# Kernel tuning notes

Hardware: AMD Instinct MI355X
Metric: run time of the kernel (lower is better)

Reference implementation:

```python
import jax, jax.numpy as jnp
import numpy as np

EMB_DIM = 1024
NUM_HEADS = 16
DEPTH = EMB_DIM // NUM_HEADS
B, LQ, LKV = 2, 1024, 2048


def setup_inputs() -> dict:
    key = jax.random.key(0)
    ks = jax.random.split(key, 8)
    s = 1.0 / np.sqrt(EMB_DIM)
    return {
        "x": jax.random.normal(ks[0], (B, LQ, EMB_DIM), jnp.float32),
        "context": jax.random.normal(ks[1], (B, LKV, EMB_DIM), jnp.float32),
        "pad_mask": jax.random.bernoulli(ks[2], 0.1, (B, LQ, LKV)),
        "Wq": jax.random.normal(ks[3], (EMB_DIM, EMB_DIM), jnp.float32) * s,
        "Wk": jax.random.normal(ks[4], (EMB_DIM, EMB_DIM), jnp.float32) * s,
        "Wv": jax.random.normal(ks[5], (EMB_DIM, EMB_DIM), jnp.float32) * s,
        "fc_w": jax.random.normal(ks[6], (EMB_DIM, EMB_DIM), jnp.float32) * s,
        "fc_b": jax.random.normal(ks[7], (EMB_DIM,), jnp.float32) * s,
    }


def reference(x, context, pad_mask, Wq, Wk, Wv, fc_w, fc_b):
    # Projections (torch Linear: y = x @ W.T)
    Q = jnp.einsum("bqe,fe->bqf", x, Wq)
    K = jnp.einsum("bke,fe->bkf", context, Wk)
    V = jnp.einsum("bke,fe->bkf", context, Wv)
    # Split heads: [B, H, L, D]
    Q = Q.reshape(B, LQ, NUM_HEADS, DEPTH).transpose(0, 2, 1, 3)
    K = K.reshape(B, LKV, NUM_HEADS, DEPTH).transpose(0, 2, 1, 3)
    V = V.reshape(B, LKV, NUM_HEADS, DEPTH).transpose(0, 2, 1, 3)
    # Scaled dot-product attention scores [B, H, LQ, LKV]
    scores = jnp.einsum("bhqd,bhkd->bhqk", Q, K) / np.sqrt(DEPTH).astype(np.float32)
    scores = jnp.where(pad_mask[:, None, :, :], jnp.float32(-1e9), scores)
    att = jax.nn.softmax(scores, axis=-1)
    out = jnp.einsum("bhqk,bhkd->bhqd", att, V)
    out = out.transpose(0, 2, 1, 3).reshape(B, LQ, EMB_DIM)
    return jnp.einsum("bqe,fe->bqf", out, fc_w) + fc_b
```

## Files before the change

### kernel.cpp

```cpp
#include <hip/hip_runtime.h>
#include <hip/hip_bf16.h>

#define B_   2
#define H_   16
#define LQ_  1024
#define LKV_ 2048
#define D_   64
#define E_   1024

typedef __attribute__((ext_vector_type(8))) _Float16 f16x8;
typedef __attribute__((ext_vector_type(4))) float   f32x4;

__device__ __forceinline__ void gload16_lds(const void* g, void* l) {
    __builtin_amdgcn_global_load_lds(
        (const __attribute__((address_space(1))) unsigned int*)g,
        (__attribute__((address_space(3))) unsigned int*)l, 16, 0, 0);
}

__global__ void probe14(const void* __restrict__ msk, int* __restrict__ modep) {
    int lane = threadIdx.x;
    int notInt = 0, notF32 = 0, notBF = 0;
    for (int i = lane; i < 256; i += 64) {
        unsigned v = ((const unsigned*)msk)[i * 997];
        if (v > 1u) notInt = 1;
        if (v != 0u && v != 0x3F800000u) notF32 = 1;
        if (v != 0u && v != 0x3F80u && v != 0x3F800000u && v != 0x3F803F80u) notBF = 1;
    }
    notInt = __any(notInt); notF32 = __any(notF32); notBF = __any(notBF);
    if (lane == 0) *modep = !notInt ? 0 : (!notF32 ? 1 : (!notBF ? 2 : 3));
}

__global__ void canon14_all(
    const float* __restrict__ x,  const float* __restrict__ ctx,
    const float* __restrict__ wq, const float* __restrict__ wk,
    const float* __restrict__ wv, const float* __restrict__ fw,
    const float* __restrict__ fb, const void* __restrict__ msk,
    _Float16* __restrict__ xh,  _Float16* __restrict__ ch,
    _Float16* __restrict__ wqh, _Float16* __restrict__ wkvh,
    _Float16* __restrict__ fwh, float* __restrict__ fbf,
    unsigned long long* __restrict__ Mbt, const int* __restrict__ modep)
{
    const int mmode = *modep;
    const int total = 1376384;
    const int stride = gridDim.x * blockDim.x;
    for (int idx = blockIdx.x * blockDim.x + threadIdx.x; idx < total; idx += stride) {
        if (idx < 1310720) {
            const float* src; _Float16* dst; int rel;
            if (idx < 262144)       { src = x;   dst = xh;   rel = idx; }
            else if (idx < 786432)  { src = ctx; dst = ch;   rel = idx - 262144; }
            else if (idx < 917504)  { src = wq;  dst = wqh;  rel = idx - 786432; }
            else if (idx < 1048576) { src = wk;  dst = wkvh; rel = idx - 917504; }
            else if (idx < 1179648) { src = wv;  dst = wkvh + (size_t)E_ * E_; rel = idx - 1048576; }
            else                    { src = fw;  dst = fwh;  rel = idx - 1179648; }
            f32x4 a = ((const f32x4*)src)[2 * rel], b = ((const f32x4*)src)[2 * rel + 1];
            f16x8 o;
            o[0] = (_Float16)a.x; o[1] = (_Float16)a.y; o[2] = (_Float16)a.z; o[3] = (_Float16)a.w;
            o[4] = (_Float16)b.x; o[5] = (_Float16)b.y; o[6] = (_Float16)b.z; o[7] = (_Float16)b.w;
            ((f16x8*)dst)[rel] = o;
        } else if (idx < 1310848) {
            int rel = idx - 1310720;
#pragma unroll
            for (int j = 0; j < 8; ++j) fbf[rel * 8 + j] = fb[rel * 8 + j];
        } else {
            int rel = idx - 1310848;
            const size_t base = (size_t)rel * 64;
            unsigned long long v = 0;
            if (mmode == 0) {
                const int* p = (const int*)msk + base;
#pragma unroll
                for (int j = 0; j < 64; ++j) if (p[j] != 0) v |= 1ull << j;
            } else if (mmode == 1) {
                const float* p = (const float*)msk + base;
#pragma unroll
                for (int j = 0; j < 64; ++j) if (p[j] != 0.0f) v |= 1ull << j;
            } else if (mmode == 2) {
                const unsigned short* p = (const unsigned short*)msk + base;
#pragma unroll
                for (int j = 0; j < 64; ++j) if (p[j] != 0) v |= 1ull << j;
            } else {
                const unsigned char* p = (const unsigned char*)msk + base;
#pragma unroll
                for (int j = 0; j < 64; ++j) if (p[j] != 0) v |= 1ull << j;
            }
            Mbt[(rel & 31) * 2048 + (rel >> 5)] = v;
        }
    }
}

__global__ __launch_bounds__(256) void gemm14_qkv(
    const _Float16* __restrict__ xh, const _Float16* __restrict__ ch,
    const _Float16* __restrict__ wqh, const _Float16* __restrict__ wkvh,
    _Float16* __restrict__ Qh, _Float16* __restrict__ Kh, _Float16* __restrict__ Vt)
{
    __shared__ __align__(16) _Float16 As[128 * 64];
    __shared__ __align__(16) _Float16 Bs[128 * 64];

    const int bid = blockIdx.x;
    const bool isQ = bid < 128;
    const _Float16* A; const _Float16* W; int tm, tn;
    if (isQ) { A = xh; W = wqh; tm = bid >> 3; tn = bid & 7; }
    else     { int b2 = bid - 128; A = ch; W = wkvh; tm = b2 >> 4; tn = b2 & 15; }

    const int tid = threadIdx.x;
    const int w = tid >> 6, lane = tid & 63;
    const int g = lane >> 4, c = lane & 15;
    const int wr = w >> 1, wc = w & 1;
    const int rowS = lane >> 3, slot = lane & 7;
    const int stSwz = ((slot ^ (rowS & 7)) << 4);
    const int swz0 = ((g ^ (c & 7)) << 4);
    const int swz1 = (((4 + g) ^ (c & 7)) << 4);

    f32x4 acc[4][4];
#pragma unroll
    for (int i = 0; i < 4; i++)
#pragma unroll
        for (int j = 0; j < 4; j++) acc[i][j] = f32x4{0.f, 0.f, 0.f, 0.f};

    const size_t rowB = (size_t)E_ * 2;
    const char* gAbase = (const char*)A + (size_t)(tm * 128) * rowB;
    const char* gBbase = (const char*)W + (size_t)(tn * 128) * rowB;

    for (int kt = 0; kt < 16; ++kt) {
#pragma unroll
        for (int j = 0; j < 4; ++j) {
            int rloc = w * 32 + j * 8 + rowS;
            gload16_lds(gAbase + (size_t)rloc * rowB + kt * 128 + stSwz,
                        (char*)As + (w * 32 + j * 8) * 128 + lane * 16);
            gload16_lds(gBbase + (size_t)rloc * rowB + kt * 128 + stSwz,
                        (char*)Bs + (w * 32 + j * 8) * 128 + lane * 16);
        }
        __syncthreads();

        f16x8 bF[4][2];
#pragma unroll
        for (int ni = 0; ni < 4; ni++) {
            const char* bp = (const char*)Bs + (wc * 64 + ni * 16 + c) * 128;
            bF[ni][0] = *(const f16x8*)(bp + swz0);
            bF[ni][1] = *(const f16x8*)(bp + swz1);
        }
#pragma unroll
        for (int mi = 0; mi < 4; mi++) {
            const char* ap = (const char*)As + (wr * 64 + mi * 16 + c) * 128;
            f16x8 a0 = *(const f16x8*)(ap + swz0);
            f16x8 a1 = *(const f16x8*)(ap + swz1);
#pragma unroll
            for (int ni = 0; ni < 4; ni++) {
                acc[mi][ni] = __builtin_amdgcn_mfma_f32_16x16x32_f16(a0, bF[ni][0], acc[mi][ni], 0, 0, 0);
                acc[mi][ni] = __builtin_amdgcn_mfma_f32_16x16x32_f16(a1, bF[ni][1], acc[mi][ni], 0, 0, 0);
            }
        }
        __syncthreads();
    }

#pragma unroll
    for (int mi = 0; mi < 4; mi++) {
#pragma unroll
        for (int ni = 0; ni < 4; ni++) {
#pragma unroll
            for (int r = 0; r < 4; r++) {
                int R  = tm * 128 + wr * 64 + mi * 16 + g * 4 + r;
                int Cc = tn * 128 + wc * 64 + ni * 16 + c;
                float v = acc[mi][ni][r];
                if (isQ) {
                    int b = R >> 10, q = R & 1023;
                    int h = Cc >> 6, d = Cc & 63;
                    Qh[((size_t)(b * H_ + h) * LQ_ + q) * D_ + d] = (_Float16)(v * 0.18033688011112042f);
                } else {
                    int b = R >> 11, k = R & 2047;
                    int isV = Cc >> 10, cc2 = Cc & 1023;
                    int h = cc2 >> 6, d = cc2 & 63;
                    if (!isV)
                        Kh[((size_t)(b * H_ + h) * LKV_ + k) * D_ + d] = (_Float16)v;
                    else {
                        size_t bh = (size_t)(b * H_ + h);
                        Vt[((bh * (LKV_ / 64) + (k >> 6)) * D_ + d) * 64 + (k & 63)] = (_Float16)v;
                    }
                }
            }
        }
    }
}

__global__ __launch_bounds__(256) void gemm14_fc(
    const _Float16* __restrict__ A, const _Float16* __restrict__ W,
    const float* __restrict__ bias, float* __restrict__ Cout)
{
    __shared__ __align__(16) _Float16 As[128 * 64];
    __shared__ __align__(16) _Float16 Bs[128 * 64];

    const int tm = blockIdx.x >> 3, tn = blockIdx.x & 7;
    const int tid = threadIdx.x;
    const int w = tid >> 6, lane = tid & 63;
    const int g = lane >> 4, c = lane & 15;
    const int wr = w >> 1, wc = w & 1;
    const int rowS = lane >> 3, slot = lane & 7;
    const int stSwz = ((slot ^ (rowS & 7)) << 4);
    const int swz0 = ((g ^ (c & 7)) << 4);
    const int swz1 = (((4 + g) ^ (c & 7)) << 4);

    f32x4 acc[4][4];
#pragma unroll
    for (int i = 0; i < 4; i++)
#pragma unroll
        for (int j = 0; j < 4; j++) acc[i][j] = f32x4{0.f, 0.f, 0.f, 0.f};

    const size_t rowB = (size_t)E_ * 2;
    const char* gAbase = (const char*)A + (size_t)(tm * 128) * rowB;
    const char* gBbase = (const char*)W + (size_t)(tn * 128) * rowB;

    for (int kt = 0; kt < 16; ++kt) {
#pragma unroll
        for (int j = 0; j < 4; ++j) {
            int rloc = w * 32 + j * 8 + rowS;
            gload16_lds(gAbase + (size_t)rloc * rowB + kt * 128 + stSwz,
                        (char*)As + (w * 32 + j * 8) * 128 + lane * 16);
            gload16_lds(gBbase + (size_t)rloc * rowB + kt * 128 + stSwz,
                        (char*)Bs + (w * 32 + j * 8) * 128 + lane * 16);
        }
        __syncthreads();

        f16x8 bF[4][2];
#pragma unroll
        for (int ni = 0; ni < 4; ni++) {
            const char* bp = (const char*)Bs + (wc * 64 + ni * 16 + c) * 128;
            bF[ni][0] = *(const f16x8*)(bp + swz0);
            bF[ni][1] = *(const f16x8*)(bp + swz1);
        }
#pragma unroll
        for (int mi = 0; mi < 4; mi++) {
            const char* ap = (const char*)As + (wr * 64 + mi * 16 + c) * 128;
            f16x8 a0 = *(const f16x8*)(ap + swz0);
            f16x8 a1 = *(const f16x8*)(ap + swz1);
#pragma unroll
            for (int ni = 0; ni < 4; ni++) {
                acc[mi][ni] = __builtin_amdgcn_mfma_f32_16x16x32_f16(a0, bF[ni][0], acc[mi][ni], 0, 0, 0);
                acc[mi][ni] = __builtin_amdgcn_mfma_f32_16x16x32_f16(a1, bF[ni][1], acc[mi][ni], 0, 0, 0);
            }
        }
        __syncthreads();
    }

#pragma unroll
    for (int mi = 0; mi < 4; mi++)
#pragma unroll
        for (int ni = 0; ni < 4; ni++)
#pragma unroll
            for (int r = 0; r < 4; r++) {
                int R  = tm * 128 + wr * 64 + mi * 16 + g * 4 + r;
                int Cc = tn * 128 + wc * 64 + ni * 16 + c;
                Cout[(size_t)R * E_ + Cc] = acc[mi][ni][r] + bias[Cc];
            }
}

__global__ __launch_bounds__(256) void attn14_kernel(
    const _Float16* __restrict__ Qh,
    const _Float16* __restrict__ Kh,
    const _Float16* __restrict__ Vt,
    const unsigned long long* __restrict__ Mbt,
    _Float16* __restrict__ O)
{
    __shared__ __align__(16) char ldsraw[32768];

    const int bid0 = blockIdx.x;
    const int xcd = bid0 & 7, jj = bid0 >> 3;
    const int bh = xcd * 4 + (jj >> 4);
    const int qt = jj & 15;
    const int b = bh >> 4, h = bh & 15;
    const int tid = threadIdx.x;
    const int w = tid >> 6, lane = tid & 63;
    const int g = lane >> 4, c = lane & 15;
    const int q0 = qt * 64 + w * 16;

    f16x8 qf[2];
#pragma unroll
    for (int ks = 0; ks < 2; ++ks)
        qf[ks] = *(const f16x8*)&Qh[((size_t)bh * LQ_ + q0 + c) * D_ + ks * 32 + g * 8];

    f32x4 o[4];
#pragma unroll
    for (int dt = 0; dt < 4; dt++) o[dt] = f32x4{0.f, 0.f, 0.f, 0.f};
    float m = -1e30f, lsum = 0.f;

    const int rowS = (lane >> 3);
    const int stOffBase = (rowS * 128) + (((lane & 7) ^ (rowS & 7)) * 16);
    const char* kTile0 = (const char*)Kh + (size_t)bh * (LKV_ * D_ * 2);
    const char* vTile0 = (const char*)Vt + (size_t)bh * (LKV_ * D_ * 2);

    int rdOff[2];
#pragma unroll
    for (int ks = 0; ks < 2; ++ks)
        rdOff[ks] = c * 128 + (((ks * 4 + g) ^ (c & 7)) * 16);

    const int srcLo = (((g & 1) << 1) * 16 + c) << 2;
    const int srcHi = ((((g & 1) << 1) + 1) * 16 + c) << 2;
    const bool hiSel = (g >= 2);

    const int mRowIdx = b * LQ_ + q0 + c;

    {
#pragma unroll
        for (int j = 0; j < 2; ++j) {
            gload16_lds(kTile0 + (w * 2048 + j * 1024) + stOffBase, ldsraw + (w * 2048 + j * 1024));
            gload16_lds(vTile0 + (w * 2048 + j * 1024) + stOffBase, ldsraw + 8192 + (w * 2048 + j * 1024));
        }
    }
    __syncthreads();

    for (int t = 0; t < 32; ++t) {
        if (t < 31) {
            const char* kt = kTile0 + (size_t)(t + 1) * 8192;
            const char* vt = vTile0 + (size_t)(t + 1) * 8192;
            char* dst = ldsraw + ((t + 1) & 1) * 16384;
#pragma unroll
            for (int j = 0; j < 2; ++j) {
                gload16_lds(kt + (w * 2048 + j * 1024) + stOffBase, dst + (w * 2048 + j * 1024));
                gload16_lds(vt + (w * 2048 + j * 1024) + stOffBase, dst + 8192 + (w * 2048 + j * 1024));
            }
        }

        const char* bufp = ldsraw + (t & 1) * 16384;

        f32x4 s[4];
#pragma unroll
        for (int nt = 0; nt < 4; ++nt) {
            f32x4 accS = f32x4{0.f, 0.f, 0.f, 0.f};
#pragma unroll
            for (int ks = 0; ks < 2; ++ks) {
                f16x8 kf = *(const f16x8*)(bufp + nt * 2048 + rdOff[ks]);
                accS = __builtin_amdgcn_mfma_f32_16x16x32_f16(kf, qf[ks], accS, 0, 0, 0);
            }
            s[nt] = accS;
        }
        unsigned long long mks = Mbt[(size_t)t * 2048 + mRowIdx] >> (g * 4);
#pragma unroll
        for (int nt = 0; nt < 4; ++nt) {
            unsigned nib = (unsigned)(mks >> (nt * 16)) & 0xFu;
            if (nib & 1u) s[nt][0] = -1e9f;
            if (nib & 2u) s[nt][1] = -1e9f;
            if (nib & 4u) s[nt][2] = -1e9f;
            if (nib & 8u) s[nt][3] = -1e9f;
        }
        float t0 = fmaxf(fmaxf(s[0][0], s[0][1]), fmaxf(s[0][2], s[0][3]));
        float t1 = fmaxf(fmaxf(s[1][0], s[1][1]), fmaxf(s[1][2], s[1][3]));
        float t2 = fmaxf(fmaxf(s[2][0], s[2][1]), fmaxf(s[2][2], s[2][3]));
        float t3 = fmaxf(fmaxf(s[3][0], s[3][1]), fmaxf(s[3][2], s[3][3]));
        float tmax = fmaxf(fmaxf(t0, t1), fmaxf(t2, t3));
        tmax = fmaxf(tmax, __shfl_xor(tmax, 16, 64));
        tmax = fmaxf(tmax, __shfl_xor(tmax, 32, 64));
        float mn = fmaxf(m, tmax);
        float scl = exp2f(m - mn);
        m = mn;
        float ts = 0.f;
#pragma unroll
        for (int nt = 0; nt < 4; ++nt) {
            float p0 = exp2f(s[nt][0] - m);
            float p1 = exp2f(s[nt][1] - m);
            float p2 = exp2f(s[nt][2] - m);
            float p3 = exp2f(s[nt][3] - m);
            s[nt][0] = p0; s[nt][1] = p1; s[nt][2] = p2; s[nt][3] = p3;
            ts += (p0 + p1) + (p2 + p3);
        }
        ts += __shfl_xor(ts, 16, 64);
        ts += __shfl_xor(ts, 32, 64);
        lsum = lsum * scl + ts;
#pragma unroll
        for (int dt = 0; dt < 4; dt++)
#pragma unroll
            for (int r = 0; r < 4; r++) o[dt][r] *= scl;
        int pk[4][2];
#pragma unroll
        for (int nt = 0; nt < 4; ++nt) {
            pk[nt][0] = __builtin_bit_cast(int, __builtin_amdgcn_cvt_pkrtz(s[nt][0], s[nt][1]));
            pk[nt][1] = __builtin_bit_cast(int, __builtin_amdgcn_cvt_pkrtz(s[nt][2], s[nt][3]));
        }
#pragma unroll
        for (int ks = 0; ks < 2; ++ks) {
            const int ntL = 2 * ks, ntH = 2 * ks + 1;
            int aL0 = __builtin_amdgcn_ds_bpermute(srcLo, pk[ntL][0]);
            int aL1 = __builtin_amdgcn_ds_bpermute(srcLo, pk[ntL][1]);
            int aH0 = __builtin_amdgcn_ds_bpermute(srcHi, pk[ntL][0]);
            int aH1 = __builtin_amdgcn_ds_bpermute(srcHi, pk[ntL][1]);
            int bL0 = __builtin_amdgcn_ds_bpermute(srcLo, pk[ntH][0]);
            int bL1 = __builtin_amdgcn_ds_bpermute(srcLo, pk[ntH][1]);
            int bH0 = __builtin_amdgcn_ds_bpermute(srcHi, pk[ntH][0]);
            int bH1 = __builtin_amdgcn_ds_bpermute(srcHi, pk[ntH][1]);
            int u[4];
            u[0] = hiSel ? bL0 : aL0;
            u[1] = hiSel ? bL1 : aL1;
            u[2] = hiSel ? bH0 : aH0;
            u[3] = hiSel ? bH1 : aH1;
            f16x8 pf;
            {
                union { int i[4]; f16x8 v; } cvt;
                cvt.i[0] = u[0]; cvt.i[1] = u[1]; cvt.i[2] = u[2]; cvt.i[3] = u[3];
                pf = cvt.v;
            }
#pragma unroll
            for (int dt = 0; dt < 4; ++dt) {
                f16x8 vf = *(const f16x8*)(bufp + 8192 + dt * 2048 + rdOff[ks]);
                o[dt] = __builtin_amdgcn_mfma_f32_16x16x32_f16(vf, pf, o[dt], 0, 0, 0);
            }
        }
        __syncthreads();
    }

    float inv = 1.0f / lsum;
    float* OfP = (float*)ldsraw;
#pragma unroll
    for (int dt = 0; dt < 4; ++dt)
#pragma unroll
        for (int r = 0; r < 4; r++)
            OfP[(w * 16 + c) * 68 + dt * 16 + 4 * g + r] = o[dt][r] * inv;
    __syncthreads();

    {
        int row = tid >> 2, seg = tid & 3;
        const float* src = &OfP[row * 68 + seg * 16];
        f16x8 lo, hi;
#pragma unroll
        for (int i = 0; i < 8; ++i) { lo[i] = (_Float16)src[i]; hi[i] = (_Float16)src[8 + i]; }
        _Float16* dst = &O[((size_t)b * LQ_ + qt * 64 + row) * E_ + h * 64 + seg * 16];
        *(f16x8*)dst = lo;
        *(f16x8*)(dst + 8) = hi;
    }
}

extern "C" void kernel_launch(void* const* d_in, const int* in_sizes, int n_in,
                              void* d_out, int out_size, void* d_ws, size_t ws_size,
                              hipStream_t stream)
{
    const float* x   = (const float*)d_in[0];
    const float* ctx = (const float*)d_in[1];
    const void*  msk = d_in[2];
    const float* Wq  = (const float*)d_in[3];
    const float* Wk  = (const float*)d_in[4];
    const float* Wv  = (const float*)d_in[5];
    const float* fcw = (const float*)d_in[6];
    const float* fcb = (const float*)d_in[7];
    float* out = (float*)d_out;

    char* ws = (char*)d_ws;
    size_t off = 0;
    auto alloc = [&](size_t bytes) { char* p = ws + off; off += (bytes + 255) & ~255ull; return p; };

    int* modep = (int*)alloc(256);
    unsigned long long* Mbt = (unsigned long long*)alloc((size_t)B_ * LQ_ * (LKV_ / 64) * 8);
    _Float16* xh   = (_Float16*)alloc((size_t)B_ * LQ_ * E_ * 2);
    _Float16* ch   = (_Float16*)alloc((size_t)B_ * LKV_ * E_ * 2);
    _Float16* wqh  = (_Float16*)alloc((size_t)E_ * E_ * 2);
    _Float16* wkvh = (_Float16*)alloc((size_t)2 * E_ * E_ * 2);
    _Float16* fwh  = (_Float16*)alloc((size_t)E_ * E_ * 2);
    float*    fbf  = (float*)alloc((size_t)E_ * 4);
    _Float16* Qh   = (_Float16*)alloc((size_t)B_ * H_ * LQ_ * D_ * 2);
    _Float16* Kh   = (_Float16*)alloc((size_t)B_ * H_ * LKV_ * D_ * 2);
    _Float16* Vt   = (_Float16*)alloc((size_t)B_ * H_ * LKV_ * D_ * 2);
    _Float16* Ob   = xh;
    (void)ws_size; (void)in_sizes; (void)n_in; (void)out_size;

    probe14<<<1, 64, 0, stream>>>(msk, modep);

    canon14_all<<<2048, 256, 0, stream>>>(x, ctx, Wq, Wk, Wv, fcw, fcb, msk,
                                          xh, ch, wqh, wkvh, fwh, fbf, Mbt, modep);

    gemm14_qkv<<<640, 256, 0, stream>>>(xh, ch, wqh, wkvh, Qh, Kh, Vt);

    attn14_kernel<<<512, 256, 0, stream>>>(Qh, Kh, Vt, Mbt, Ob);

    gemm14_fc<<<128, 256, 0, stream>>>(Ob, fwh, fbf, out);
}
```

Baseline: 151.0 us.

## Split attention KV range across two wave groups and merge partial softmax

The attention block grows to 512 threads: two groups of four waves each process half of the KV sequence (16 tiles each) in separate LDS halves. The partial outputs, maxima and sums are combined in LDS at the end. The online-softmax rescale is also skipped unless the max grows by more than a threshold, which removes most per-tile exp and rescale work. This doubles waves per block and LDS use (64KB) for more parallelism per query tile, at the cost of a merge step and lower block occupancy per CU.

```diff
diff --git a/kernel.cpp b/kernel.cpp
--- a/kernel.cpp
+++ b/kernel.cpp
@@ -17,7 +17,7 @@
         (__attribute__((address_space(3))) unsigned int*)l, 16, 0, 0);
 }
 
-__global__ void probe14(const void* __restrict__ msk, int* __restrict__ modep) {
+__global__ void probe15(const void* __restrict__ msk, int* __restrict__ modep) {
     int lane = threadIdx.x;
     int notInt = 0, notF32 = 0, notBF = 0;
     for (int i = lane; i < 256; i += 64) {
@@ -30,7 +30,7 @@
     if (lane == 0) *modep = !notInt ? 0 : (!notF32 ? 1 : (!notBF ? 2 : 3));
 }
 
-__global__ void canon14_all(
+__global__ void canon15_all(
     const float* __restrict__ x,  const float* __restrict__ ctx,
     const float* __restrict__ wq, const float* __restrict__ wk,
     const float* __restrict__ wv, const float* __restrict__ fw,
@@ -87,7 +87,7 @@
     }
 }
 
-__global__ __launch_bounds__(256) void gemm14_qkv(
+__global__ __launch_bounds__(256) void gemm15_qkv(
     const _Float16* __restrict__ xh, const _Float16* __restrict__ ch,
     const _Float16* __restrict__ wqh, const _Float16* __restrict__ wkvh,
     _Float16* __restrict__ Qh, _Float16* __restrict__ Kh, _Float16* __restrict__ Vt)
@@ -181,7 +181,7 @@
     }
 }
 
-__global__ __launch_bounds__(256) void gemm14_fc(
+__global__ __launch_bounds__(256) void gemm15_fc(
     const _Float16* __restrict__ A, const _Float16* __restrict__ W,
     const float* __restrict__ bias, float* __restrict__ Cout)
 {
@@ -252,14 +252,14 @@
             }
 }
 
-__global__ __launch_bounds__(256) void attn14_kernel(
+__global__ __launch_bounds__(512) void attn15_kernel(
     const _Float16* __restrict__ Qh,
     const _Float16* __restrict__ Kh,
     const _Float16* __restrict__ Vt,
     const unsigned long long* __restrict__ Mbt,
     _Float16* __restrict__ O)
 {
-    __shared__ __align__(16) char ldsraw[32768];
+    __shared__ __align__(16) char ldsraw[65536];
 
     const int bid0 = blockIdx.x;
     const int xcd = bid0 & 7, jj = bid0 >> 3;
@@ -269,7 +269,10 @@
     const int tid = threadIdx.x;
     const int w = tid >> 6, lane = tid & 63;
     const int g = lane >> 4, c = lane & 15;
-    const int q0 = qt * 64 + w * 16;
+    const int ws = w >> 2, wq = w & 3;
+    const int q0 = qt * 64 + wq * 16;
+
+    char* half = ldsraw + ws * 32768;
 
     f16x8 qf[2];
 #pragma unroll
@@ -283,8 +286,8 @@
 
     const int rowS = (lane >> 3);
     const int stOffBase = (rowS * 128) + (((lane & 7) ^ (rowS & 7)) * 16);
-    const char* kTile0 = (const char*)Kh + (size_t)bh * (LKV_ * D_ * 2);
-    const char* vTile0 = (const char*)Vt + (size_t)bh * (LKV_ * D_ * 2);
+    const char* kTileB = (const char*)Kh + (size_t)bh * (LKV_ * D_ * 2) + (size_t)ws * 16 * 8192;
+    const char* vTileB = (const char*)Vt + (size_t)bh * (LKV_ * D_ * 2) + (size_t)ws * 16 * 8192;
 
     int rdOff[2];
 #pragma unroll
@@ -296,29 +299,30 @@
     const bool hiSel = (g >= 2);
 
     const int mRowIdx = b * LQ_ + q0 + c;
+    const size_t mTile0 = (size_t)(ws * 16) * 2048 + mRowIdx;
 
     {
 #pragma unroll
         for (int j = 0; j < 2; ++j) {
-            gload16_lds(kTile0 + (w * 2048 + j * 1024) + stOffBase, ldsraw + (w * 2048 + j * 1024));
-            gload16_lds(vTile0 + (w * 2048 + j * 1024) + stOffBase, ldsraw + 8192 + (w * 2048 + j * 1024));
+            gload16_lds(kTileB + (wq * 2048 + j * 1024) + stOffBase, half + (wq * 2048 + j * 1024));
+            gload16_lds(vTileB + (wq * 2048 + j * 1024) + stOffBase, half + 8192 + (wq * 2048 + j * 1024));
         }
     }
     __syncthreads();
 
-    for (int t = 0; t < 32; ++t) {
-        if (t < 31) {
-            const char* kt = kTile0 + (size_t)(t + 1) * 8192;
-            const char* vt = vTile0 + (size_t)(t + 1) * 8192;
-            char* dst = ldsraw + ((t + 1) & 1) * 16384;
+    for (int t = 0; t < 16; ++t) {
+        if (t < 15) {
+            const char* kt = kTileB + (size_t)(t + 1) * 8192;
+            const char* vt = vTileB + (size_t)(t + 1) * 8192;
+            char* dst = half + ((t + 1) & 1) * 16384;
 #pragma unroll
             for (int j = 0; j < 2; ++j) {
-                gload16_lds(kt + (w * 2048 + j * 1024) + stOffBase, dst + (w * 2048 + j * 1024));
-                gload16_lds(vt + (w * 2048 + j * 1024) + stOffBase, dst + 8192 + (w * 2048 + j * 1024));
-            }
-        }
-
-        const char* bufp = ldsraw + (t & 1) * 16384;
+                gload16_lds(kt + (wq * 2048 + j * 1024) + stOffBase, dst + (wq * 2048 + j * 1024));
+                gload16_lds(vt + (wq * 2048 + j * 1024) + stOffBase, dst + 8192 + (wq * 2048 + j * 1024));
+            }
+        }
+
+        const char* bufp = half + (t & 1) * 16384;
 
         f32x4 s[4];
 #pragma unroll
@@ -331,7 +335,7 @@
             }
             s[nt] = accS;
         }
-        unsigned long long mks = Mbt[(size_t)t * 2048 + mRowIdx] >> (g * 4);
+        unsigned long long mks = Mbt[mTile0 + (size_t)t * 2048] >> (g * 4);
 #pragma unroll
         for (int nt = 0; nt < 4; ++nt) {
             unsigned nib = (unsigned)(mks >> (nt * 16)) & 0xFu;
@@ -347,9 +351,16 @@
         float tmax = fmaxf(fmaxf(t0, t1), fmaxf(t2, t3));
         tmax = fmaxf(tmax, __shfl_xor(tmax, 16, 64));
         tmax = fmaxf(tmax, __shfl_xor(tmax, 32, 64));
-        float mn = fmaxf(m, tmax);
-        float scl = exp2f(m - mn);
-        m = mn;
+        if (!__all(tmax - m <= 8.0f)) {
+            float mn = fmaxf(m, tmax);
+            float scl = exp2f(m - mn);
+            m = mn;
+            lsum *= scl;
+#pragma unroll
+            for (int dt = 0; dt < 4; dt++)
+#pragma unroll
+                for (int r = 0; r < 4; r++) o[dt][r] *= scl;
+        }
         float ts = 0.f;
 #pragma unroll
         for (int nt = 0; nt < 4; ++nt) {
@@ -362,11 +373,7 @@
         }
         ts += __shfl_xor(ts, 16, 64);
         ts += __shfl_xor(ts, 32, 64);
-        lsum = lsum * scl + ts;
-#pragma unroll
-        for (int dt = 0; dt < 4; dt++)
-#pragma unroll
-            for (int r = 0; r < 4; r++) o[dt][r] *= scl;
+        lsum += ts;
         int pk[4][2];
 #pragma unroll
         for (int nt = 0; nt < 4; ++nt) {
@@ -404,24 +411,31 @@
         __syncthreads();
     }
 
-    float inv = 1.0f / lsum;
     float* OfP = (float*)ldsraw;
+    float* Ml  = (float*)(ldsraw + 34816);
 #pragma unroll
     for (int dt = 0; dt < 4; ++dt)
 #pragma unroll
         for (int r = 0; r < 4; r++)
-            OfP[(w * 16 + c) * 68 + dt * 16 + 4 * g + r] = o[dt][r] * inv;
+            OfP[(w * 16 + c) * 68 + dt * 16 + 4 * g + r] = o[dt][r];
+    if (lane < 16) {
+        Ml[(w * 16 + lane) * 2 + 0] = m;
+        Ml[(w * 16 + lane) * 2 + 1] = lsum;
+    }
     __syncthreads();
 
-    {
-        int row = tid >> 2, seg = tid & 3;
-        const float* src = &OfP[row * 68 + seg * 16];
-        f16x8 lo, hi;
-#pragma unroll
-        for (int i = 0; i < 8; ++i) { lo[i] = (_Float16)src[i]; hi[i] = (_Float16)src[8 + i]; }
-        _Float16* dst = &O[((size_t)b * LQ_ + qt * 64 + row) * E_ + h * 64 + seg * 16];
-        *(f16x8*)dst = lo;
-        *(f16x8*)(dst + 8) = hi;
+    const int d = tid & 63;
+    const int qlBase = tid >> 6;
+#pragma unroll
+    for (int pass = 0; pass < 8; ++pass) {
+        int ql = pass * 8 + qlBase;
+        float m0 = Ml[ql * 2], l0 = Ml[ql * 2 + 1];
+        float m1 = Ml[(64 + ql) * 2], l1 = Ml[(64 + ql) * 2 + 1];
+        float M  = fmaxf(m0, m1);
+        float e0 = exp2f(m0 - M), e1 = exp2f(m1 - M);
+        float L  = l0 * e0 + l1 * e1;
+        float acc = OfP[ql * 68 + d] * e0 + OfP[(64 + ql) * 68 + d] * e1;
+        O[((size_t)b * LQ_ + qt * 64 + ql) * E_ + h * 64 + d] = (_Float16)(acc / L);
     }
 }
 
@@ -457,14 +471,14 @@
     _Float16* Ob   = xh;
     (void)ws_size; (void)in_sizes; (void)n_in; (void)out_size;
 
-    probe14<<<1, 64, 0, stream>>>(msk, modep);
-
-    canon14_all<<<2048, 256, 0, stream>>>(x, ctx, Wq, Wk, Wv, fcw, fcb, msk,
+    probe15<<<1, 64, 0, stream>>>(msk, modep);
+
+    canon15_all<<<2048, 256, 0, stream>>>(x, ctx, Wq, Wk, Wv, fcw, fcb, msk,
                                           xh, ch, wqh, wkvh, fwh, fbf, Mbt, modep);
 
-    gemm14_qkv<<<640, 256, 0, stream>>>(xh, ch, wqh, wkvh, Qh, Kh, Vt);
-
-    attn14_kernel<<<512, 256, 0, stream>>>(Qh, Kh, Vt, Mbt, Ob);
-
-    gemm14_fc<<<128, 256, 0, stream>>>(Ob, fwh, fbf, out);
-}
+    gemm15_qkv<<<640, 256, 0, stream>>>(xh, ch, wqh, wkvh, Qh, Kh, Vt);
+
+    attn15_kernel<<<512, 512, 0, stream>>>(Qh, Kh, Vt, Mbt, Ob);
+
+    gemm15_fc<<<128, 256, 0, stream>>>(Ob, fwh, fbf, out);
+}
```

After: 143.4 us. 5.0% less time.
